# Kernel tuning notes

Measured on AMD Instinct MI355X. Metric: run time of the kernel, lower is better.

## Reference

```python
import jax, jax.numpy as jnp
import numpy as np
import math

D_MODEL, NHEAD, N_LAYERS = 128, 8, 4
LAYER_NAMES = ("self", "cross", "self", "cross")
B, H, W = 2, 128, 160
MID = D_MODEL
D_FF = 2 * D_MODEL
BN_EPS = 1e-5
LN_EPS = 1e-5
ATTN_EPS = 1e-6


def setup_inputs() -> dict:
    key = jax.random.key(0)
    ks = iter(jax.random.split(key, 64))

    def rn(shape, scale):
        return jax.random.normal(next(ks), shape, dtype=jnp.float32) * scale

    inp = {}
    inp["ref_feature"] = rn((B, D_MODEL, H, W), 1.0)
    inp["src_feature"] = rn((B, D_MODEL, H, W), 1.0)
    K = np.array([[200.0, 0.0, W / 2.0], [0.0, 200.0, H / 2.0], [0.0, 0.0, 1.0]], np.float32)

    def make_proj(tx):
        E = np.eye(4, dtype=np.float32); E[0, 3] = tx
        P = np.eye(4, dtype=np.float32); P[:3, :4] = K @ E[:3, :4]
        return np.broadcast_to(P, (B, 4, 4)).astype(np.float32).copy()

    rp, sp = make_proj(0.0), make_proj(10.0)
    inp["ref_proj"] = jnp.asarray(rp)
    inp["src_proj"] = jnp.asarray(sp)
    inp["ref_img2world"] = jnp.asarray(np.linalg.inv(rp))
    inp["src_img2world"] = jnp.asarray(np.linalg.inv(sp))
    inp["depth_hypo"] = 500.0 + 100.0 * jax.random.uniform(next(ks), (B, 1, H, W), dtype=jnp.float32)
    xav = 0.08  # ~xavier std for 128x128
    inp["attn_w"] = rn((N_LAYERS, 4, D_MODEL, D_MODEL), xav)  # q,k,v,out
    inp["attn_b"] = jnp.zeros((N_LAYERS, 4, D_MODEL), jnp.float32)
    inp["ffn_w1"] = rn((N_LAYERS, D_MODEL, D_FF), 0.07)
    inp["ffn_b1"] = jnp.zeros((N_LAYERS, D_FF), jnp.float32)
    inp["ffn_w2"] = rn((N_LAYERS, D_FF, D_MODEL), 0.07)
    inp["ffn_b2"] = jnp.zeros((N_LAYERS, D_MODEL), jnp.float32)
    inp["ln_g"] = jnp.ones((N_LAYERS, 2, D_MODEL), jnp.float32)
    inp["ln_b"] = jnp.zeros((N_LAYERS, 2, D_MODEL), jnp.float32)
    inp["rc_w"] = rn((MID, 1, 3, 3), 0.01)
    inp["rc_b"] = jnp.zeros((MID,), jnp.float32)
    inp["bn2_g"] = jnp.ones((MID,), jnp.float32)
    inp["bn2_b"] = jnp.zeros((MID,), jnp.float32)
    inp["cc_w"] = rn((MID, D_MODEL), xav)
    inp["cc_b"] = jnp.zeros((D_MODEL,), jnp.float32)
    inp["bn1_g"] = jnp.ones((16,), jnp.float32)
    inp["bn1_b"] = jnp.zeros((16,), jnp.float32)
    inp["fc1_w"] = rn((16, MID), 0.16)
    inp["fc1_b"] = jnp.zeros((MID,), jnp.float32)
    inp["fc2_w"] = rn((MID, MID), xav)
    inp["fc2_b"] = jnp.zeros((MID,), jnp.float32)
    inp["ser_w"] = rn((MID, MID), xav)
    inp["ser_b"] = jnp.zeros((MID,), jnp.float32)
    inp["see_w"] = rn((MID, MID), xav)
    inp["see_b"] = jnp.zeros((MID,), jnp.float32)
    return inp


def sine_pe(d_model, Hh, Ww):
    # PositionEncodingSine (temp_bug_fix=True), computed only on the [H,W] slice
    y_pos = jnp.arange(1, Hh + 1, dtype=jnp.float32)[:, None] * jnp.ones((1, Ww), jnp.float32)
    x_pos = jnp.ones((Hh, 1), jnp.float32) * jnp.arange(1, Ww + 1, dtype=jnp.float32)[None, :]
    div = jnp.exp(jnp.arange(0, d_model // 2, 2, dtype=jnp.float32) * (-math.log(10000.0) / (d_model // 2)))[:, None, None]
    pe = jnp.stack([jnp.sin(x_pos * div), jnp.cos(x_pos * div), jnp.sin(y_pos * div), jnp.cos(y_pos * div)], axis=1)
    return pe.reshape(d_model, Hh, Ww)


def grid_sample_bilinear(feat, grid):
    # feat [B,C,Hs,Ws], grid [B,P,2] normalized to [-1,1]; align_corners=True, zeros padding
    Bn, C, Hs, Ws = feat.shape
    P = grid.shape[1]
    x = (grid[..., 0] + 1.0) * 0.5 * (Ws - 1)
    y = (grid[..., 1] + 1.0) * 0.5 * (Hs - 1)
    x0, y0 = jnp.floor(x), jnp.floor(y)
    wx, wy = x - x0, y - y0
    flat = feat.reshape(Bn, C, Hs * Ws)

    def gather(xi, yi):
        valid = (xi >= 0) & (xi <= Ws - 1) & (yi >= 0) & (yi <= Hs - 1)
        xi_c = jnp.clip(xi, 0, Ws - 1).astype(jnp.int32)
        yi_c = jnp.clip(yi, 0, Hs - 1).astype(jnp.int32)
        idx = yi_c * Ws + xi_c  # [B,P]
        v = jnp.take_along_axis(flat, jnp.broadcast_to(idx[:, None, :], (Bn, C, P)), axis=2)
        return v * valid[:, None, :].astype(feat.dtype)

    v00 = gather(x0, y0)
    v01 = gather(x0 + 1, y0)
    v10 = gather(x0, y0 + 1)
    v11 = gather(x0 + 1, y0 + 1)
    wx, wy = wx[:, None, :], wy[:, None, :]
    return v00 * (1 - wx) * (1 - wy) + v01 * wx * (1 - wy) + v10 * (1 - wx) * wy + v11 * wx * wy


def homo_warp_ref_to_src(feat, ref_proj, src_proj, depth):
    # homo_warping_pe with fea='ref': proj = ref_proj @ inv(src_proj)
    Bn, C, Hs, Ws = feat.shape
    _, D, Hr, Wr = depth.shape
    proj = jnp.einsum('bij,bjk->bik', ref_proj, jnp.linalg.inv(src_proj))
    rot, trans = proj[:, :3, :3], proj[:, :3, 3]
    yy, xx = jnp.meshgrid(jnp.arange(Hr, dtype=jnp.float32), jnp.arange(Wr, dtype=jnp.float32), indexing='ij')
    xyz = jnp.stack([xx.ravel(), yy.ravel(), jnp.ones(Hr * Wr, jnp.float32)], 0)  # [3, P]
    rot_xyz = jnp.einsum('bij,jp->bip', rot, xyz)  # [B,3,P]
    pxyz = rot_xyz[:, :, None, :] * depth.reshape(Bn, 1, D, Hr * Wr) + trans[:, :, None, None]
    z = pxyz[:, 2]
    z = jnp.where(z == 0, 1e-9, z)
    gx = (pxyz[:, 0] / z) / ((Ws - 1) / 2.0) - 1.0
    gy = (pxyz[:, 1] / z) / ((Hs - 1) / 2.0) - 1.0
    grid = jax.lax.stop_gradient(jnp.stack([gx, gy], -1).reshape(Bn, D * Hr * Wr, 2))  # torch no_grad
    out = grid_sample_bilinear(feat, grid)
    return out.reshape(Bn, C, D, Hr, Wr)


def layer_norm(x, g, b):
    mu = x.mean(-1, keepdims=True)
    var = ((x - mu) ** 2).mean(-1, keepdims=True)
    return (x - mu) * jax.lax.rsqrt(var + LN_EPS) * g + b


def encoder_layer(x, src, w, bb, w1, b1f, w2, b2f, g, bt):
    N, L, d = x.shape
    h, dh = NHEAD, d // NHEAD
    q = (x @ w[0] + bb[0]).reshape(N, L, h, dh)
    k = (src @ w[1] + bb[1]).reshape(N, -1, h, dh)
    v = (src @ w[2] + bb[2]).reshape(N, -1, h, dh)
    Q = jax.nn.elu(q) + 1.0
    K = jax.nn.elu(k) + 1.0
    KV = jnp.einsum('nshd,nshm->nhmd', K, v)
    Z = 1.0 / (jnp.einsum('nlhd,nhd->nlh', Q, K.sum(1)) + ATTN_EPS)
    V = jnp.einsum('nlhd,nhmd,nlh->nlhm', Q, KV, Z).reshape(N, L, d)
    x = x + (V @ w[3] + bb[3])
    x = layer_norm(x, g[0], bt[0])
    y = jax.nn.relu(x @ w1 + b1f) @ w2 + b2f
    return layer_norm(x + y, g[1], bt[1])


def cam_encode(feat, cam16, rc_w, rc_b, bn2_g, bn2_b, cc_w, cc_b, bn1_g, bn1_b,
               fc1_w, fc1_b, fc2_w, fc2_b, ser_w, ser_b, see_w, see_b):
    inv_std = 1.0 / jnp.sqrt(1.0 + BN_EPS)  # eval-mode BN, running stats (0,1)
    mlp_in = cam16 * inv_std * bn1_g + bn1_b
    hmap = jax.lax.conv_general_dilated(feat, rc_w, (1, 1), 'SAME', dimension_numbers=('NCHW', 'OIHW', 'NCHW')) + rc_b[None, :, None, None]
    hmap = jax.nn.relu(hmap * inv_std * bn2_g[None, :, None, None] + bn2_b[None, :, None, None])
    se = jax.nn.relu(mlp_in @ fc1_w + fc1_b) @ fc2_w + fc2_b  # [B, MID]
    gate = jax.nn.sigmoid(jax.nn.relu(se @ ser_w + ser_b) @ see_w + see_b)
    ctx = hmap * gate[:, :, None, None]
    return jnp.einsum('bchw,co->bohw', ctx, cc_w) + cc_b[None, :, None, None]


def reference(ref_feature, src_feature, ref_img2world, src_img2world, ref_proj, src_proj, depth_hypo,
              attn_w, attn_b, ffn_w1, ffn_b1, ffn_w2, ffn_b2, ln_g, ln_b,
              rc_w, rc_b, bn2_g, bn2_b, cc_w, cc_b, bn1_g, bn1_b,
              fc1_w, fc1_b, fc2_w, fc2_b, ser_w, ser_b, see_w, see_b):
    Bn, C, Hh, Ww = ref_feature.shape
    pe = sine_pe(C, Hh, Ww)[None]
    ref_ctx = cam_encode(depth_hypo, ref_img2world.reshape(Bn, 16), rc_w, rc_b, bn2_g, bn2_b,
                         cc_w, cc_b, bn1_g, bn1_b, fc1_w, fc1_b, fc2_w, fc2_b,
                         ser_w, ser_b, see_w, see_b)
    src_ctx = homo_warp_ref_to_src(ref_ctx, ref_proj, src_proj, depth_hypo)[:, :, 0]
    ref = (ref_feature + pe + ref_ctx).reshape(Bn, C, Hh * Ww).transpose(0, 2, 1)
    src = (src_feature + pe + src_ctx).reshape(Bn, C, Hh * Ww).transpose(0, 2, 1)
    for i, name in enumerate(LAYER_NAMES):
        p = (attn_w[i], attn_b[i], ffn_w1[i], ffn_b1[i], ffn_w2[i], ffn_b2[i], ln_g[i], ln_b[i])
        if name == 'self':
            ref = encoder_layer(ref, ref, *p)
            src = encoder_layer(src, src, *p)
        else:
            ref = encoder_layer(ref, src, *p)
            src = encoder_layer(src, ref, *p)
    return jnp.stack([ref, src])  # [2, B, H*W, C]
```

## Files before the change

kernel.cpp:

```cpp
#include <hip/hip_runtime.h>
#include <math.h>

#define BN 2
#define HH 128
#define WW 160
#define HWn (HH*WW)
#define CD 128
#define TT (BN*HWn)
#define TOKN ((size_t)TT*CD)

typedef __attribute__((ext_vector_type(8))) short bf16x8;
typedef __attribute__((ext_vector_type(4))) float f32x4;
typedef __attribute__((ext_vector_type(4))) unsigned short u16x4;

__device__ __forceinline__ float b2f(unsigned short s){
  unsigned u = ((unsigned)s) << 16;
  return __builtin_bit_cast(float, u);
}
__device__ __forceinline__ unsigned short f2b(float f){
  unsigned u = __builtin_bit_cast(unsigned, f);
  u = (u + 0x7fffu + ((u >> 16) & 1u)) >> 16;
  return (unsigned short)u;
}

__global__ __launch_bounds__(256) void k_wconv(const float* __restrict__ attn_w,
      const float* __restrict__ ffn_w1, const float* __restrict__ ffn_w2,
      const float* __restrict__ cc_w, unsigned short* __restrict__ wt,
      const float* __restrict__ ref_proj, const float* __restrict__ src_i2w,
      const float* __restrict__ cam16,
      const float* __restrict__ bn1_g, const float* __restrict__ bn1_b,
      const float* __restrict__ fc1_w, const float* __restrict__ fc1_b,
      const float* __restrict__ fc2_w, const float* __restrict__ fc2_b,
      const float* __restrict__ ser_w, const float* __restrict__ ser_b,
      const float* __restrict__ see_w, const float* __restrict__ see_b,
      float* __restrict__ projsmall, float* __restrict__ gate){
  if (blockIdx.x == 2112){
    __shared__ float mi[BN][16], t1[BN][128], t2[BN][128];
    int tid = threadIdx.x;
    const float inv_std = rsqrtf(1.0f + 1e-5f);
    if (tid < 32){
      int b = tid >> 4, idx = tid & 15, i = idx >> 2, k = idx & 3;
      float acc = 0.f;
      for (int j = 0; j < 4; j++) acc += ref_proj[b*16 + i*4 + j] * src_i2w[b*16 + j*4 + k];
      if (i < 3 && k < 3) projsmall[b*12 + i*3 + k] = acc;
      if (i < 3 && k == 3) projsmall[b*12 + 9 + i] = acc;
      mi[b][idx] = cam16[b*16 + idx] * inv_std * bn1_g[idx] + bn1_b[idx];
    }
    __syncthreads();
    int b = tid >> 7, c = tid & 127;
    float a = 0.f;
    for (int j = 0; j < 16; j++) a += mi[b][j] * fc1_w[j*128 + c];
    t1[b][c] = fmaxf(a + fc1_b[c], 0.f);
    __syncthreads();
    a = 0.f;
    for (int k = 0; k < 128; k++) a += t1[b][k] * fc2_w[k*128 + c];
    t2[b][c] = a + fc2_b[c];
    __syncthreads();
    a = 0.f;
    for (int k = 0; k < 128; k++) a += t2[b][k] * ser_w[k*128 + c];
    t1[b][c] = fmaxf(a + ser_b[c], 0.f);
    __syncthreads();
    a = 0.f;
    for (int k = 0; k < 128; k++) a += t1[b][k] * see_w[k*128 + c];
    a += see_b[c];
    gate[b*128 + c] = 1.f / (1.f + __expf(-a));
    return;
  }
  int i = blockIdx.x*256 + threadIdx.x;
  float v;
  if (i < 262144){
    int k = i & 127, n = (i >> 7) & 127, lm = i >> 14;
    v = attn_w[((size_t)lm*128 + k)*128 + n];
  } else if (i < 393216){ int j = i - 262144;
    int k = j & 127, n = (j >> 7) & 255, l = j >> 15;
    v = ffn_w1[((size_t)l*128 + k)*256 + n];
  } else if (i < 524288){ int j = i - 393216;
    int k = j & 255, n = (j >> 8) & 127, l = j >> 15;
    v = ffn_w2[((size_t)l*256 + k)*128 + n];
  } else if (i < 540672){ int j = i - 524288;
    int k = j & 127, n = j >> 7;
    v = cc_w[(size_t)k*128 + n];
  } else return;
  wt[i] = f2b(v);
}

__global__ __launch_bounds__(128) void k_hmap(const float* __restrict__ depth,
                       const float* __restrict__ rc_w, const float* __restrict__ rc_b,
                       const float* __restrict__ bn2_g, const float* __restrict__ bn2_b,
                       const float* __restrict__ gate, unsigned short* __restrict__ G){
  int bi = blockIdx.x; int n = bi / HWn; int p = bi - n*HWn;
  int y = p / WW, x = p - y*WW;
  int c = threadIdx.x;
  const float inv_std = rsqrtf(1.f + 1e-5f);
  float acc = 0.f;
#pragma unroll
  for (int ky = 0; ky < 3; ky++){
    int yy = y + ky - 1;
#pragma unroll
    for (int kx = 0; kx < 3; kx++){
      int xx = x + kx - 1;
      float v = (yy >= 0 && yy < HH && xx >= 0 && xx < WW) ? depth[n*HWn + yy*WW + xx] : 0.f;
      acc += v * rc_w[c*9 + ky*3 + kx];
    }
  }
  acc += rc_b[c];
  acc = fmaxf(acc * inv_std * bn2_g[c] + bn2_b[c], 0.f);
  G[(size_t)bi*128 + c] = f2b(acc * gate[n*128 + c]);
}

template<int K, int ACT, int LN>
__global__ __launch_bounds__(256) void k_bgemm6(
    const unsigned short* __restrict__ A, const unsigned short* __restrict__ A2, int ldA,
    const unsigned short* __restrict__ Wt,
    const float* __restrict__ bias, int amask,
    const unsigned short* __restrict__ resid,
    unsigned short* __restrict__ Cbase, size_t secStride, int ldC,
    const float* __restrict__ lng, const float* __restrict__ lnb,
    float* zfin, int zn){
  __shared__ unsigned short Wl[128*128];
  constexpr int NH = K/128;
  int tid = threadIdx.x;
  int wid = tid >> 6, lane = tid & 63;
  int sec = blockIdx.y;
  if (zfin && blockIdx.x == 0 && sec == 0){
    for (int i = tid; i < zn; i += 256) zfin[i] = 0.f;
  }
  const unsigned short* Ab = (sec == 0) ? A : A2;
  const unsigned short* Ws = Wt + (size_t)sec*128*K;
  const float* bs = bias + sec*128;
  unsigned short* C = Cbase + (size_t)sec*secStride;
  int r = lane & 15, ks = lane >> 4;
  size_t t0 = (size_t)blockIdx.x*64 + wid*16;
  const unsigned short* ap = Ab + (t0 + r)*ldA + ks*8;
  f32x4 acc[8] = {};
#pragma unroll
  for (int hh = 0; hh < NH; hh++){
    if (hh > 0) __syncthreads();
#pragma unroll
    for (int i = 0; i < 8; i++){
      int idx = i*256 + tid;
      int row = idx >> 4, c8 = idx & 15;
      int c8s = c8 ^ (row & 7);
      *(bf16x8*)&Wl[row*128 + c8s*8] = *(const bf16x8*)(Ws + (size_t)row*K + hh*128 + c8*8);
    }
    __syncthreads();
#pragma unroll
    for (int j = 0; j < 4; j++){
      bf16x8 a = *(const bf16x8*)(ap + hh*128 + j*32);
#pragma unroll
      for (int f = 0; f < 8; f++){
        int row = f*16 + r;
        int c8s = (j*4 + ks) ^ (row & 7);
        bf16x8 w = *(const bf16x8*)&Wl[row*128 + c8s*8];
        acc[f] = __builtin_amdgcn_mfma_f32_16x16x32_bf16(w, a, acc[f], 0, 0, 0);
      }
    }
  }
  bool act = (amask >> sec) & 1;
  size_t trow = t0 + r;
  float vv[8][4];
#pragma unroll
  for (int f = 0; f < 8; f++){
    float4 bi4 = *(const float4*)&bs[f*16 + 4*ks];
    vv[f][0] = acc[f][0] + bi4.x; vv[f][1] = acc[f][1] + bi4.y;
    vv[f][2] = acc[f][2] + bi4.z; vv[f][3] = acc[f][3] + bi4.w;
    if (resid){
      u16x4 rr = *(const u16x4*)(resid + trow*128 + f*16 + 4*ks);
#pragma unroll
      for (int e = 0; e < 4; e++) vv[f][e] += b2f(rr[e]);
    }
    if (act){
#pragma unroll
      for (int e = 0; e < 4; e++){
        float x = vv[f][e];
        if (ACT == 1) x = fmaxf(x, 0.f);
        if (ACT == 2) x = x > 0.f ? x + 1.f : __expf(x);
        vv[f][e] = x;
      }
    }
  }
  if (LN){
    float s = 0.f;
#pragma unroll
    for (int f = 0; f < 8; f++) s += vv[f][0]+vv[f][1]+vv[f][2]+vv[f][3];
    s += __shfl_xor(s, 16, 64); s += __shfl_xor(s, 32, 64);
    float mean = s * (1.f/128.f);
    float q = 0.f;
#pragma unroll
    for (int f = 0; f < 8; f++)
#pragma unroll
      for (int e = 0; e < 4; e++){ float d = vv[f][e]-mean; q += d*d; }
    q += __shfl_xor(q, 16, 64); q += __shfl_xor(q, 32, 64);
    float rstd = rsqrtf(q*(1.f/128.f) + 1e-5f);
#pragma unroll
    for (int f = 0; f < 8; f++){
      float4 g4 = *(const float4*)&lng[f*16 + 4*ks];
      float4 b4 = *(const float4*)&lnb[f*16 + 4*ks];
      vv[f][0] = (vv[f][0]-mean)*rstd*g4.x + b4.x;
      vv[f][1] = (vv[f][1]-mean)*rstd*g4.y + b4.y;
      vv[f][2] = (vv[f][2]-mean)*rstd*g4.z + b4.z;
      vv[f][3] = (vv[f][3]-mean)*rstd*g4.w + b4.w;
    }
  }
#pragma unroll
  for (int f = 0; f < 8; f++){
    u16x4 o;
#pragma unroll
    for (int e = 0; e < 4; e++) o[e] = f2b(vv[f][e]);
    *(u16x4*)(C + trow*ldC + f*16 + 4*ks) = o;
  }
}

__global__ __launch_bounds__(256) void k_fattnffn(
    const unsigned short* __restrict__ Q, const unsigned short* __restrict__ X,
    const float* __restrict__ kvfin, const unsigned short* __restrict__ W3,
    const float* __restrict__ b3, const float* __restrict__ g0, const float* __restrict__ b0,
    const unsigned short* __restrict__ W1t, const float* __restrict__ b1,
    const unsigned short* __restrict__ W2t, const float* __restrict__ b2,
    const float* __restrict__ g1, const float* __restrict__ lb1,
    unsigned short* __restrict__ Out, float* __restrict__ OutF){
  __shared__ unsigned short Wl[128*128];
  __shared__ unsigned short UB[64*136];
  __shared__ float ksums[8][16];
  int tid = threadIdx.x;
  size_t tb = (size_t)blockIdx.x*64;
  int g = (int)(tb / HWn);
  const float* kvb = kvfin + g*2176;
  {
    int row = tid >> 1, half = tid & 1;
    int h = row >> 4, m = row & 15;
    int swz = row & 7;
#pragma unroll
    for (int c8i = 0; c8i < 8; c8i++){
      int c8 = half*8 + c8i;
      bf16x8 val = {};
      if ((c8 >> 1) == h){
        int d0 = (c8 & 1)*8;
        const float* src = kvb + h*272 + m*16 + d0;
#pragma unroll
        for (int e = 0; e < 8; e++) ((unsigned short*)&val)[e] = f2b(src[e]);
      }
      *(bf16x8*)&Wl[row*128 + (c8 ^ swz)*8] = val;
    }
  }
  if (tid < 128) ksums[tid >> 4][tid & 15] = kvb[(tid >> 4)*272 + 256 + (tid & 15)];
  __syncthreads();
  int wid = tid >> 6, lane = tid & 63;
  int r = lane & 15, ks = lane >> 4;
  int tl = wid*16 + r;
  size_t trow = tb + tl;
  f32x4 acc[8] = {};
  float part0 = 0.f, part1 = 0.f, part2 = 0.f, part3 = 0.f;
  int myp = ks >> 1;
  int dlo = (ks & 1)*8;
#pragma unroll
  for (int j = 0; j < 4; j++){
    bf16x8 a = *(const bf16x8*)(Q + trow*128 + j*32 + ks*8);
    float pj = 0.f;
    int hj = 2*j + myp;
#pragma unroll
    for (int e = 0; e < 8; e++)
      pj += b2f(((unsigned short*)&a)[e]) * ksums[hj][dlo + e];
    if (j == 0) part0 = pj; else if (j == 1) part1 = pj;
    else if (j == 2) part2 = pj; else part3 = pj;
#pragma unroll
    for (int f = 0; f < 8; f++){
      int row = f*16 + r;
      int c8s = (j*4 + ks) ^ (row & 7);
      bf16x8 w = *(const bf16x8*)&Wl[row*128 + c8s*8];
      acc[f] = __builtin_amdgcn_mfma_f32_16x16x32_bf16(w, a, acc[f], 0, 0, 0);
    }
  }
  float full0 = part0 + __shfl_xor(part0, 16, 64);
  float full1 = part1 + __shfl_xor(part1, 16, 64);
  float full2 = part2 + __shfl_xor(part2, 16, 64);
  float full3 = part3 + __shfl_xor(part3, 16, 64);
  float oth0 = __shfl_xor(full0, 32, 64);
  float oth1 = __shfl_xor(full1, 32, 64);
  float oth2 = __shfl_xor(full2, 32, 64);
  float oth3 = __shfl_xor(full3, 32, 64);
#pragma unroll
  for (int f = 0; f < 8; f++){
    float fl, ot;
    if (f < 2){ fl = full0; ot = oth0; } else if (f < 4){ fl = full1; ot = oth1; }
    else if (f < 6){ fl = full2; ot = oth2; } else { fl = full3; ot = oth3; }
    float den = ((f & 1) == myp) ? fl : ot;
    float rc = 1.f / (den + 1e-6f);
    u16x4 o;
#pragma unroll
    for (int e = 0; e < 4; e++) o[e] = f2b(acc[f][e] * rc);
    *(u16x4*)&UB[tl*136 + f*16 + 4*ks] = o;
  }
  __syncthreads();
#pragma unroll
  for (int i = 0; i < 8; i++){
    int idx = i*256 + tid;
    int row = idx >> 4, c8 = idx & 15;
    int c8s = c8 ^ (row & 7);
    *(bf16x8*)&Wl[row*128 + c8s*8] = *(const bf16x8*)(W3 + (size_t)row*128 + c8*8);
  }
  __syncthreads();
  f32x4 acc2[8] = {};
#pragma unroll
  for (int j = 0; j < 4; j++){
    bf16x8 a = *(const bf16x8*)&UB[tl*136 + j*32 + ks*8];
#pragma unroll
    for (int f = 0; f < 8; f++){
      int row = f*16 + r;
      int c8s = (j*4 + ks) ^ (row & 7);
      bf16x8 w = *(const bf16x8*)&Wl[row*128 + c8s*8];
      acc2[f] = __builtin_amdgcn_mfma_f32_16x16x32_bf16(w, a, acc2[f], 0, 0, 0);
    }
  }
  float vv[8][4];
#pragma unroll
  for (int f = 0; f < 8; f++){
    float4 bi4 = *(const float4*)&b3[f*16 + 4*ks];
    u16x4 rr = *(const u16x4*)(X + trow*128 + f*16 + 4*ks);
    vv[f][0] = acc2[f][0] + bi4.x + b2f(rr[0]);
    vv[f][1] = acc2[f][1] + bi4.y + b2f(rr[1]);
    vv[f][2] = acc2[f][2] + bi4.z + b2f(rr[2]);
    vv[f][3] = acc2[f][3] + bi4.w + b2f(rr[3]);
  }
  {
    float s = 0.f;
#pragma unroll
    for (int f = 0; f < 8; f++) s += vv[f][0]+vv[f][1]+vv[f][2]+vv[f][3];
    s += __shfl_xor(s, 16, 64); s += __shfl_xor(s, 32, 64);
    float mean = s * (1.f/128.f);
    float q = 0.f;
#pragma unroll
    for (int f = 0; f < 8; f++)
#pragma unroll
      for (int e = 0; e < 4; e++){ float d = vv[f][e]-mean; q += d*d; }
    q += __shfl_xor(q, 16, 64); q += __shfl_xor(q, 32, 64);
    float rstd = rsqrtf(q*(1.f/128.f) + 1e-5f);
#pragma unroll
    for (int f = 0; f < 8; f++){
      float4 g4 = *(const float4*)&g0[f*16 + 4*ks];
      float4 b4 = *(const float4*)&b0[f*16 + 4*ks];
      vv[f][0] = (vv[f][0]-mean)*rstd*g4.x + b4.x;
      vv[f][1] = (vv[f][1]-mean)*rstd*g4.y + b4.y;
      vv[f][2] = (vv[f][2]-mean)*rstd*g4.z + b4.z;
      vv[f][3] = (vv[f][3]-mean)*rstd*g4.w + b4.w;
    }
  }
  u16x4 xr[8];
#pragma unroll
  for (int f = 0; f < 8; f++){
#pragma unroll
    for (int e = 0; e < 4; e++) xr[f][e] = f2b(vv[f][e]);
    *(u16x4*)&UB[tl*136 + f*16 + 4*ks] = xr[f];
  }
  __syncthreads();
  bf16x8 areg[4];
#pragma unroll
  for (int j = 0; j < 4; j++) areg[j] = *(const bf16x8*)&UB[tl*136 + j*32 + ks*8];
  f32x4 acc3[8] = {};
#pragma unroll
  for (int hh = 0; hh < 2; hh++){
    if (hh > 0) __syncthreads();
#pragma unroll
    for (int i = 0; i < 8; i++){
      int idx = i*256 + tid;
      int row = idx >> 4, c8 = idx & 15;
      *(bf16x8*)&Wl[row*128 + (c8 ^ (row & 7))*8] =
          *(const bf16x8*)(W1t + (size_t)(hh*128 + row)*128 + c8*8);
    }
    __syncthreads();
    f32x4 accf[8] = {};
#pragma unroll
    for (int j = 0; j < 4; j++){
#pragma unroll
      for (int f = 0; f < 8; f++){
        int row = f*16 + r;
        int c8s = (j*4 + ks) ^ (row & 7);
        bf16x8 w = *(const bf16x8*)&Wl[row*128 + c8s*8];
        accf[f] = __builtin_amdgcn_mfma_f32_16x16x32_bf16(w, areg[j], accf[f], 0, 0, 0);
      }
    }
#pragma unroll
    for (int f = 0; f < 8; f++){
      float4 bi4 = *(const float4*)&b1[hh*128 + f*16 + 4*ks];
      u16x4 o;
      o[0] = f2b(fmaxf(accf[f][0] + bi4.x, 0.f));
      o[1] = f2b(fmaxf(accf[f][1] + bi4.y, 0.f));
      o[2] = f2b(fmaxf(accf[f][2] + bi4.z, 0.f));
      o[3] = f2b(fmaxf(accf[f][3] + bi4.w, 0.f));
      *(u16x4*)&UB[tl*136 + f*16 + 4*ks] = o;
    }
    __syncthreads();
#pragma unroll
    for (int i = 0; i < 8; i++){
      int idx = i*256 + tid;
      int row = idx >> 4, c8 = idx & 15;
      *(bf16x8*)&Wl[row*128 + (c8 ^ (row & 7))*8] =
          *(const bf16x8*)(W2t + (size_t)row*256 + hh*128 + c8*8);
    }
    __syncthreads();
#pragma unroll
    for (int j = 0; j < 4; j++){
      bf16x8 a = *(const bf16x8*)&UB[tl*136 + j*32 + ks*8];
#pragma unroll
      for (int f = 0; f < 8; f++){
        int row = f*16 + r;
        int c8s = (j*4 + ks) ^ (row & 7);
        bf16x8 w = *(const bf16x8*)&Wl[row*128 + c8s*8];
        acc3[f] = __builtin_amdgcn_mfma_f32_16x16x32_bf16(w, a, acc3[f], 0, 0, 0);
      }
    }
  }
#pragma unroll
  for (int f = 0; f < 8; f++){
    float4 bi4 = *(const float4*)&b2[f*16 + 4*ks];
    vv[f][0] = acc3[f][0] + bi4.x + b2f(xr[f][0]);
    vv[f][1] = acc3[f][1] + bi4.y + b2f(xr[f][1]);
    vv[f][2] = acc3[f][2] + bi4.z + b2f(xr[f][2]);
    vv[f][3] = acc3[f][3] + bi4.w + b2f(xr[f][3]);
  }
  float s = 0.f;
#pragma unroll
  for (int f = 0; f < 8; f++) s += vv[f][0]+vv[f][1]+vv[f][2]+vv[f][3];
  s += __shfl_xor(s, 16, 64); s += __shfl_xor(s, 32, 64);
  float mean = s * (1.f/128.f);
  float q = 0.f;
#pragma unroll
  for (int f = 0; f < 8; f++)
#pragma unroll
    for (int e = 0; e < 4; e++){ float d = vv[f][e]-mean; q += d*d; }
  q += __shfl_xor(q, 16, 64); q += __shfl_xor(q, 32, 64);
  float rstd = rsqrtf(q*(1.f/128.f) + 1e-5f);
#pragma unroll
  for (int f = 0; f < 8; f++){
    float o0 = (vv[f][0]-mean)*rstd* g1[f*16 + 4*ks + 0] + lb1[f*16 + 4*ks + 0];
    float o1 = (vv[f][1]-mean)*rstd* g1[f*16 + 4*ks + 1] + lb1[f*16 + 4*ks + 1];
    float o2 = (vv[f][2]-mean)*rstd* g1[f*16 + 4*ks + 2] + lb1[f*16 + 4*ks + 2];
    float o3 = (vv[f][3]-mean)*rstd* g1[f*16 + 4*ks + 3] + lb1[f*16 + 4*ks + 3];
    if (Out){
      u16x4 o = { f2b(o0), f2b(o1), f2b(o2), f2b(o3) };
      *(u16x4*)(Out + trow*128 + f*16 + 4*ks) = o;
    }
    if (OutF){
      float4 of = { o0, o1, o2, o3 };
      *(float4*)(OutF + trow*128 + f*16 + 4*ks) = of;
    }
  }
}

__global__ __launch_bounds__(256) void k_kvpart(const unsigned short* __restrict__ Kb,
                         const unsigned short* __restrict__ Vb, float* __restrict__ fin){
  __shared__ float Ks[16][260], Vs[16][260];
  int bi = blockIdx.x;
  int chunk = bi % 80; int h = (bi / 80) & 7; int g = bi / 640;
  int s0 = chunk * 256;
  int tid = threadIdx.x;
#pragma unroll
  for (int rr = 0; rr < 8; rr++){
    int idx = rr*256 + tid;
    int s = idx >> 3, d2 = idx & 7;
    size_t gg = ((size_t)(g*HWn + s0 + s))*128 + h*16 + d2*2;
    Ks[d2*2  ][s] = b2f(Kb[gg]);
    Ks[d2*2+1][s] = b2f(Kb[gg+1]);
    Vs[d2*2  ][s] = b2f(Vb[gg]);
    Vs[d2*2+1][s] = b2f(Vb[gg+1]);
  }
  __syncthreads();
  int m = tid >> 4, d = tid & 15;
  float acc = 0.f, ksum = 0.f;
#pragma unroll 4
  for (int s4 = 0; s4 < 64; s4++){
    float4 kv = *(const float4*)&Ks[d][s4*4];
    float4 vv = *(const float4*)&Vs[m][s4*4];
    acc  += kv.x*vv.x + kv.y*vv.y + kv.z*vv.z + kv.w*vv.w;
    ksum += kv.x + kv.y + kv.z + kv.w;
  }
  float* fb = fin + (size_t)(g*8 + h)*272;
  atomicAdd(&fb[tid], acc);
  if (m == 0) atomicAdd(&fb[256 + d], ksum);
}

__global__ __launch_bounds__(128) void k_warp(const unsigned short* __restrict__ ctxref,
     const float* __restrict__ depth, const float* __restrict__ projs,
     unsigned short* __restrict__ ctxsrc){
  int bi = blockIdx.x; int n = bi / HWn; int p = bi - n*HWn;
  int y = p / WW, x = p - y*WW;
  const float* pr = &projs[n*12];
  float d = depth[n*HWn + p];
  float fx = (float)x, fy = (float)y;
  float px = (pr[0]*fx + pr[1]*fy + pr[2])*d + pr[9];
  float py = (pr[3]*fx + pr[4]*fy + pr[5])*d + pr[10];
  float pz = (pr[6]*fx + pr[7]*fy + pr[8])*d + pr[11];
  if (pz == 0.f) pz = 1e-9f;
  float xs = px/pz, ys = py/pz;
  float x0 = floorf(xs), y0 = floorf(ys);
  float wx = xs - x0, wy = ys - y0;
  int c = threadIdx.x;
  float acc = 0.f;
#pragma unroll
  for (int dy = 0; dy < 2; dy++){
    float cy = y0 + dy;
    float wyv = dy ? wy : 1.f - wy;
#pragma unroll
    for (int dx = 0; dx < 2; dx++){
      float cx = x0 + dx;
      float wxv = dx ? wx : 1.f - wx;
      bool valid = (cx >= 0.f) && (cx <= (float)(WW-1)) && (cy >= 0.f) && (cy <= (float)(HH-1));
      int xi = (int)fminf(fmaxf(cx, 0.f), (float)(WW-1));
      int yi = (int)fminf(fmaxf(cy, 0.f), (float)(HH-1));
      float v = b2f(ctxref[((size_t)(n*HWn) + yi*WW + xi)*128 + c]);
      acc += valid ? wxv*wyv*v : 0.f;
    }
  }
  ctxsrc[(size_t)bi*128 + c] = f2b(acc);
}

__global__ __launch_bounds__(256) void k_build2(const float* __restrict__ featR,
      const float* __restrict__ featS,
      const unsigned short* __restrict__ ctxR, const unsigned short* __restrict__ ctxS,
      unsigned short* __restrict__ outR, unsigned short* __restrict__ outS){
  __shared__ float tile[32][33];
  int tx = threadIdx.x, ty = threadIdx.y;
  int z = blockIdx.z; int b = z & (BN-1); int sel = z >> 1;
  const float* feat = sel ? featS : featR;
  const unsigned short* ctx = sel ? ctxS : ctxR;
  unsigned short* out = sel ? outS : outR;
  int p0 = blockIdx.x*32, c0 = blockIdx.y*32;
  for (int i = ty; i < 32; i += 8)
    tile[i][tx] = feat[((size_t)(b*CD + c0 + i))*HWn + p0 + tx];
  __syncthreads();
  const float LOG1E4_32 = 0.28782313662425572f;
  for (int r = ty; r < 32; r += 8){
    int p = p0 + r, c = c0 + tx;
    int y = p / WW, x = p - y*WW;
    int i = c >> 2, j = c & 3;
    float dv = __expf(-(float)i * LOG1E4_32);
    float pos = (j < 2) ? (float)(x + 1) : (float)(y + 1);
    float arg = pos * dv;
    float pe = (j & 1) ? cosf(arg) : sinf(arg);
    size_t o = ((size_t)(b*HWn) + p)*128 + c;
    out[o] = f2b(tile[tx][r] + pe + b2f(ctx[o]));
  }
}

extern "C" void kernel_launch(void* const* d_in, const int* in_sizes, int n_in,
                              void* d_out, int out_size, void* d_ws, size_t ws_size,
                              hipStream_t stream) {
  const float* ref_feature = (const float*)d_in[0];
  const float* src_feature = (const float*)d_in[1];
  const float* ref_proj    = (const float*)d_in[2];
  const float* ref_i2w     = (const float*)d_in[4];
  const float* src_i2w     = (const float*)d_in[5];
  const float* depth       = (const float*)d_in[6];
  const float* attn_w      = (const float*)d_in[7];
  const float* attn_b      = (const float*)d_in[8];
  const float* ffn_w1      = (const float*)d_in[9];
  const float* ffn_b1      = (const float*)d_in[10];
  const float* ffn_w2      = (const float*)d_in[11];
  const float* ffn_b2      = (const float*)d_in[12];
  const float* ln_g        = (const float*)d_in[13];
  const float* ln_b        = (const float*)d_in[14];
  const float* rc_w        = (const float*)d_in[15];
  const float* rc_b        = (const float*)d_in[16];
  const float* bn2_g       = (const float*)d_in[17];
  const float* bn2_b       = (const float*)d_in[18];
  const float* cc_w        = (const float*)d_in[19];
  const float* cc_b        = (const float*)d_in[20];
  const float* bn1_g       = (const float*)d_in[21];
  const float* bn1_b       = (const float*)d_in[22];
  const float* fc1_w       = (const float*)d_in[23];
  const float* fc1_b       = (const float*)d_in[24];
  const float* fc2_w       = (const float*)d_in[25];
  const float* fc2_b       = (const float*)d_in[26];
  const float* ser_w       = (const float*)d_in[27];
  const float* ser_b       = (const float*)d_in[28];
  const float* see_w       = (const float*)d_in[29];
  const float* see_b       = (const float*)d_in[30];

  const size_t small_f32 = (size_t)4*2176 + 32 + 256;
  const size_t small_bytes = small_f32*4 + (size_t)540672*2 + 4096;
  const size_t need_batch = (size_t)TOKN*2*8 + small_bytes;
  bool BATCH = ws_size >= need_batch;
  const size_t CSEG = BATCH ? 2*TOKN : TOKN;

  char* p = (char*)d_ws;
  unsigned short* Rm = (unsigned short*)p; p += TOKN*2;
  unsigned short* Sm = (unsigned short*)p; p += TOKN*2;
  unsigned short* QB = (unsigned short*)p; p += CSEG*3*2;
  unsigned short* KB = QB + CSEG;
  unsigned short* VB = QB + 2*CSEG;
  float* KVFIN  = (float*)p; p += (size_t)(BATCH?4:2)*2176*4;
  float* PROJ   = (float*)p; p += 32*4;
  float* GATE   = (float*)p; p += 256*4;
  unsigned short* WT = (unsigned short*)p;

  float* OUT = (float*)d_out;

  k_wconv<<<2113, 256, 0, stream>>>(attn_w, ffn_w1, ffn_w2, cc_w, WT,
      ref_proj, src_i2w, ref_i2w, bn1_g, bn1_b, fc1_w, fc1_b,
      fc2_w, fc2_b, ser_w, ser_b, see_w, see_b, PROJ, GATE);
  k_hmap<<<TT, 128, 0, stream>>>(depth, rc_w, rc_b, bn2_g, bn2_b, GATE, QB);
  k_bgemm6<128,0,0><<<dim3(TT/64, 1), 256, 0, stream>>>(
      QB, QB, 128, WT + 524288, cc_b, 0, nullptr, KB, 0, 128, nullptr, nullptr,
      nullptr, 0);
  k_warp<<<TT, 128, 0, stream>>>(KB, depth, PROJ, VB);
  k_build2<<<dim3(HWn/32, 4, 2*BN), dim3(32, 8), 0, stream>>>(
      ref_feature, src_feature, KB, VB, Rm, Sm);

  auto encode = [&](unsigned short* x, const unsigned short* srcp, int l, int nTok,
                    unsigned short* outBf, float* outF){
    const unsigned short* ATW = WT + (size_t)l*65536;
    const unsigned short* F1T = WT + 262144 + (size_t)l*32768;
    const unsigned short* F2T = WT + 393216 + (size_t)l*32768;
    const float* Bv = attn_b + (size_t)l*512;
    const float* g0 = ln_g + (size_t)l*256; const float* b0 = ln_b + (size_t)l*256;
    int nb = nTok/64, ng = nTok/HWn;
    k_bgemm6<128,2,0><<<dim3(nb, 3), 256, 0, stream>>>(x, srcp, 128, ATW, Bv, 0b011,
                                              nullptr, QB, CSEG, 128, nullptr, nullptr,
                                              KVFIN, ng*2176);
    k_kvpart<<<ng*640, 256, 0, stream>>>(KB, VB, KVFIN);
    k_fattnffn<<<nb, 256, 0, stream>>>(QB, x, KVFIN, ATW + 3*16384, Bv + 384, g0, b0,
                                       F1T, ffn_b1 + (size_t)l*256, F2T,
                                       ffn_b2 + (size_t)l*128, g0 + 128, b0 + 128,
                                       outBf, outF);
  };

  if (BATCH) encode(Rm, Rm, 0, 2*TT, Rm, nullptr);
  else { encode(Rm, Rm, 0, TT, Rm, nullptr); encode(Sm, Sm, 0, TT, Sm, nullptr); }
  encode(Rm, Sm, 1, TT, Rm, nullptr); encode(Sm, Rm, 1, TT, Sm, nullptr);
  if (BATCH) encode(Rm, Rm, 2, 2*TT, Rm, nullptr);
  else { encode(Rm, Rm, 2, TT, Rm, nullptr); encode(Sm, Sm, 2, TT, Sm, nullptr); }
  encode(Rm, Sm, 3, TT, Rm, OUT);
  encode(Sm, Rm, 3, TT, nullptr, OUT + TOKN);
}
```

Measured before the change: 551.8 us.

## Fuse QKV projection with KV reduction and double-buffer KV accumulator zeroing

Replaces the three-section QKV GEMM and separate kvpart reduction with one kernel. It computes Q, K and V per 64-token tile, keeps K and V in shared memory, and atomically accumulates the per-head K^T V and K sums. This removes writing and re-reading the K/V buffers and saves a launch per layer. The KV accumulator is now double-buffered and zeroed by the previous attention/FFN kernel, with the initial zeroing done in the weight-conversion kernel. The trade-off is more serialized work per block and contention from many global atomics.

```diff
diff --git a/kernel.cpp b/kernel.cpp
--- a/kernel.cpp
+++ b/kernel.cpp
@@ -33,7 +33,12 @@
       const float* __restrict__ fc2_w, const float* __restrict__ fc2_b,
       const float* __restrict__ ser_w, const float* __restrict__ ser_b,
       const float* __restrict__ see_w, const float* __restrict__ see_b,
-      float* __restrict__ projsmall, float* __restrict__ gate){
+      float* __restrict__ projsmall, float* __restrict__ gate,
+      float* __restrict__ kvz, int kvn){
+  if (blockIdx.x == 2113){
+    for (int i = threadIdx.x; i < kvn; i += 256) kvz[i] = 0.f;
+    return;
+  }
   if (blockIdx.x == 2112){
     __shared__ float mi[BN][16], t1[BN][128], t2[BN][128];
     int tid = threadIdx.x;
@@ -115,16 +120,12 @@
     const float* __restrict__ bias, int amask,
     const unsigned short* __restrict__ resid,
     unsigned short* __restrict__ Cbase, size_t secStride, int ldC,
-    const float* __restrict__ lng, const float* __restrict__ lnb,
-    float* zfin, int zn){
+    const float* __restrict__ lng, const float* __restrict__ lnb){
   __shared__ unsigned short Wl[128*128];
   constexpr int NH = K/128;
   int tid = threadIdx.x;
   int wid = tid >> 6, lane = tid & 63;
   int sec = blockIdx.y;
-  if (zfin && blockIdx.x == 0 && sec == 0){
-    for (int i = tid; i < zn; i += 256) zfin[i] = 0.f;
-  }
   const unsigned short* Ab = (sec == 0) ? A : A2;
   const unsigned short* Ws = Wt + (size_t)sec*128*K;
   const float* bs = bias + sec*128;
@@ -211,6 +212,144 @@
   }
 }
 
+__global__ __launch_bounds__(256) void k_qkv(
+    const unsigned short* __restrict__ X, const unsigned short* __restrict__ S,
+    const unsigned short* __restrict__ Wt,
+    const float* __restrict__ bias,
+    unsigned short* __restrict__ QB, float* __restrict__ kvfin){
+  __shared__ unsigned short Wl[128*128];
+  __shared__ unsigned short Kl[64*136];
+  int tid = threadIdx.x;
+  int wid = tid >> 6, lane = tid & 63;
+  int r = lane & 15, ks = lane >> 4;
+  size_t t0 = (size_t)blockIdx.x*64 + wid*16;
+  int tl = wid*16 + r;
+  size_t trow = t0 + r;
+  int g = (int)(((size_t)blockIdx.x*64) / HWn);
+  bf16x8 ax[4], as_[4];
+#pragma unroll
+  for (int j = 0; j < 4; j++){
+    ax[j]  = *(const bf16x8*)(X + trow*128 + j*32 + ks*8);
+    as_[j] = *(const bf16x8*)(S + trow*128 + j*32 + ks*8);
+  }
+#pragma unroll
+  for (int i = 0; i < 8; i++){
+    int idx = i*256 + tid;
+    int row = idx >> 4, c8 = idx & 15;
+    *(bf16x8*)&Wl[row*128 + (c8 ^ (row & 7))*8] = *(const bf16x8*)(Wt + (size_t)row*128 + c8*8);
+  }
+  __syncthreads();
+  {
+    f32x4 acc[8] = {};
+#pragma unroll
+    for (int j = 0; j < 4; j++)
+#pragma unroll
+      for (int f = 0; f < 8; f++){
+        int row = f*16 + r;
+        bf16x8 w = *(const bf16x8*)&Wl[row*128 + ((j*4 + ks) ^ (row & 7))*8];
+        acc[f] = __builtin_amdgcn_mfma_f32_16x16x32_bf16(w, ax[j], acc[f], 0, 0, 0);
+      }
+    __syncthreads();
+#pragma unroll
+    for (int i = 0; i < 8; i++){
+      int idx = i*256 + tid;
+      int row = idx >> 4, c8 = idx & 15;
+      *(bf16x8*)&Wl[row*128 + (c8 ^ (row & 7))*8] =
+          *(const bf16x8*)(Wt + 16384 + (size_t)row*128 + c8*8);
+    }
+#pragma unroll
+    for (int f = 0; f < 8; f++){
+      float4 b4 = *(const float4*)&bias[f*16 + 4*ks];
+      u16x4 o;
+#pragma unroll
+      for (int e = 0; e < 4; e++){
+        float x = acc[f][e] + ((const float*)&b4)[e];
+        x = x > 0.f ? x + 1.f : __expf(x);
+        o[e] = f2b(x);
+      }
+      *(u16x4*)(QB + trow*128 + f*16 + 4*ks) = o;
+    }
+  }
+  __syncthreads();
+  {
+    f32x4 acc[8] = {};
+#pragma unroll
+    for (int j = 0; j < 4; j++)
+#pragma unroll
+      for (int f = 0; f < 8; f++){
+        int row = f*16 + r;
+        bf16x8 w = *(const bf16x8*)&Wl[row*128 + ((j*4 + ks) ^ (row & 7))*8];
+        acc[f] = __builtin_amdgcn_mfma_f32_16x16x32_bf16(w, as_[j], acc[f], 0, 0, 0);
+      }
+    __syncthreads();
+#pragma unroll
+    for (int i = 0; i < 8; i++){
+      int idx = i*256 + tid;
+      int row = idx >> 4, c8 = idx & 15;
+      *(bf16x8*)&Wl[row*128 + (c8 ^ (row & 7))*8] =
+          *(const bf16x8*)(Wt + 32768 + (size_t)row*128 + c8*8);
+    }
+#pragma unroll
+    for (int f = 0; f < 8; f++){
+      float4 b4 = *(const float4*)&bias[128 + f*16 + 4*ks];
+      u16x4 o;
+#pragma unroll
+      for (int e = 0; e < 4; e++){
+        float x = acc[f][e] + ((const float*)&b4)[e];
+        x = x > 0.f ? x + 1.f : __expf(x);
+        o[e] = f2b(x);
+      }
+      *(u16x4*)&Kl[tl*136 + f*16 + 4*ks] = o;
+    }
+  }
+  __syncthreads();
+  {
+    f32x4 acc[8] = {};
+#pragma unroll
+    for (int j = 0; j < 4; j++)
+#pragma unroll
+      for (int f = 0; f < 8; f++){
+        int row = f*16 + r;
+        bf16x8 w = *(const bf16x8*)&Wl[row*128 + ((j*4 + ks) ^ (row & 7))*8];
+        acc[f] = __builtin_amdgcn_mfma_f32_16x16x32_bf16(w, as_[j], acc[f], 0, 0, 0);
+      }
+    __syncthreads();
+    unsigned short* Vl = Wl;
+#pragma unroll
+    for (int f = 0; f < 8; f++){
+      float4 b4 = *(const float4*)&bias[256 + f*16 + 4*ks];
+      u16x4 o;
+#pragma unroll
+      for (int e = 0; e < 4; e++) o[e] = f2b(acc[f][e] + ((const float*)&b4)[e]);
+      *(u16x4*)&Vl[tl*136 + f*16 + 4*ks] = o;
+    }
+  }
+  __syncthreads();
+  {
+    const unsigned short* Vl = Wl;
+    int h = tid >> 5, m = (tid >> 1) & 15, db = (tid & 1)*8;
+    float a8[8] = {}; float ksc[8] = {};
+#pragma unroll 4
+    for (int t = 0; t < 64; t++){
+      float vv_ = b2f(Vl[t*136 + h*16 + m]);
+      bf16x8 kk = *(const bf16x8*)&Kl[t*136 + h*16 + db];
+#pragma unroll
+      for (int c = 0; c < 8; c++){
+        float kf = b2f(((unsigned short*)&kk)[c]);
+        a8[c] += kf * vv_;
+        ksc[c] += kf;
+      }
+    }
+    float* fb = kvfin + (size_t)g*2176 + h*272;
+#pragma unroll
+    for (int c = 0; c < 8; c++) atomicAdd(fb + m*16 + db + c, a8[c]);
+    if (m == 0){
+#pragma unroll
+      for (int c = 0; c < 8; c++) atomicAdd(fb + 256 + db + c, ksc[c]);
+    }
+  }
+}
+
 __global__ __launch_bounds__(256) void k_fattnffn(
     const unsigned short* __restrict__ Q, const unsigned short* __restrict__ X,
     const float* __restrict__ kvfin, const unsigned short* __restrict__ W3,
@@ -218,11 +357,15 @@
     const unsigned short* __restrict__ W1t, const float* __restrict__ b1,
     const unsigned short* __restrict__ W2t, const float* __restrict__ b2,
     const float* __restrict__ g1, const float* __restrict__ lb1,
-    unsigned short* __restrict__ Out, float* __restrict__ OutF){
+    unsigned short* __restrict__ Out, float* __restrict__ OutF,
+    float* zeroNext, int zn){
   __shared__ unsigned short Wl[128*128];
   __shared__ unsigned short UB[64*136];
   __shared__ float ksums[8][16];
   int tid = threadIdx.x;
+  if (zeroNext && blockIdx.x == 0){
+    for (int i = tid; i < zn; i += 256) zeroNext[i] = 0.f;
+  }
   size_t tb = (size_t)blockIdx.x*64;
   int g = (int)(tb / HWn);
   const float* kvb = kvfin + g*2176;
@@ -432,10 +575,12 @@
   float rstd = rsqrtf(q*(1.f/128.f) + 1e-5f);
 #pragma unroll
   for (int f = 0; f < 8; f++){
-    float o0 = (vv[f][0]-mean)*rstd* g1[f*16 + 4*ks + 0] + lb1[f*16 + 4*ks + 0];
-    float o1 = (vv[f][1]-mean)*rstd* g1[f*16 + 4*ks + 1] + lb1[f*16 + 4*ks + 1];
-    float o2 = (vv[f][2]-mean)*rstd* g1[f*16 + 4*ks + 2] + lb1[f*16 + 4*ks + 2];
-    float o3 = (vv[f][3]-mean)*rstd* g1[f*16 + 4*ks + 3] + lb1[f*16 + 4*ks + 3];
+    float4 g4 = *(const float4*)&g1[f*16 + 4*ks];
+    float4 b4 = *(const float4*)&lb1[f*16 + 4*ks];
+    float o0 = (vv[f][0]-mean)*rstd*g4.x + b4.x;
+    float o1 = (vv[f][1]-mean)*rstd*g4.y + b4.y;
+    float o2 = (vv[f][2]-mean)*rstd*g4.z + b4.z;
+    float o3 = (vv[f][3]-mean)*rstd*g4.w + b4.w;
     if (Out){
       u16x4 o = { f2b(o0), f2b(o1), f2b(o2), f2b(o3) };
       *(u16x4*)(Out + trow*128 + f*16 + 4*ks) = o;
@@ -445,38 +590,6 @@
       *(float4*)(OutF + trow*128 + f*16 + 4*ks) = of;
     }
   }
-}
-
-__global__ __launch_bounds__(256) void k_kvpart(const unsigned short* __restrict__ Kb,
-                         const unsigned short* __restrict__ Vb, float* __restrict__ fin){
-  __shared__ float Ks[16][260], Vs[16][260];
-  int bi = blockIdx.x;
-  int chunk = bi % 80; int h = (bi / 80) & 7; int g = bi / 640;
-  int s0 = chunk * 256;
-  int tid = threadIdx.x;
-#pragma unroll
-  for (int rr = 0; rr < 8; rr++){
-    int idx = rr*256 + tid;
-    int s = idx >> 3, d2 = idx & 7;
-    size_t gg = ((size_t)(g*HWn + s0 + s))*128 + h*16 + d2*2;
-    Ks[d2*2  ][s] = b2f(Kb[gg]);
-    Ks[d2*2+1][s] = b2f(Kb[gg+1]);
-    Vs[d2*2  ][s] = b2f(Vb[gg]);
-    Vs[d2*2+1][s] = b2f(Vb[gg+1]);
-  }
-  __syncthreads();
-  int m = tid >> 4, d = tid & 15;
-  float acc = 0.f, ksum = 0.f;
-#pragma unroll 4
-  for (int s4 = 0; s4 < 64; s4++){
-    float4 kv = *(const float4*)&Ks[d][s4*4];
-    float4 vv = *(const float4*)&Vs[m][s4*4];
-    acc  += kv.x*vv.x + kv.y*vv.y + kv.z*vv.z + kv.w*vv.w;
-    ksum += kv.x + kv.y + kv.z + kv.w;
-  }
-  float* fb = fin + (size_t)(g*8 + h)*272;
-  atomicAdd(&fb[tid], acc);
-  if (m == 0) atomicAdd(&fb[256 + d], ksum);
 }
 
 __global__ __launch_bounds__(128) void k_warp(const unsigned short* __restrict__ ctxref,
@@ -576,7 +689,7 @@
   const float* see_w       = (const float*)d_in[29];
   const float* see_b       = (const float*)d_in[30];
 
-  const size_t small_f32 = (size_t)4*2176 + 32 + 256;
+  const size_t small_f32 = (size_t)2*4*2176 + 32 + 256;
   const size_t small_bytes = small_f32*4 + (size_t)540672*2 + 4096;
   const size_t need_batch = (size_t)TOKN*2*8 + small_bytes;
   bool BATCH = ws_size >= need_batch;
@@ -588,24 +701,25 @@
   unsigned short* QB = (unsigned short*)p; p += CSEG*3*2;
   unsigned short* KB = QB + CSEG;
   unsigned short* VB = QB + 2*CSEG;
-  float* KVFIN  = (float*)p; p += (size_t)(BATCH?4:2)*2176*4;
+  float* KVFIN  = (float*)p; p += (size_t)2*4*2176*4;
   float* PROJ   = (float*)p; p += 32*4;
   float* GATE   = (float*)p; p += 256*4;
   unsigned short* WT = (unsigned short*)p;
 
   float* OUT = (float*)d_out;
 
-  k_wconv<<<2113, 256, 0, stream>>>(attn_w, ffn_w1, ffn_w2, cc_w, WT,
+  k_wconv<<<2114, 256, 0, stream>>>(attn_w, ffn_w1, ffn_w2, cc_w, WT,
       ref_proj, src_i2w, ref_i2w, bn1_g, bn1_b, fc1_w, fc1_b,
-      fc2_w, fc2_b, ser_w, ser_b, see_w, see_b, PROJ, GATE);
+      fc2_w, fc2_b, ser_w, ser_b, see_w, see_b, PROJ, GATE,
+      KVFIN, 2*4*2176);
   k_hmap<<<TT, 128, 0, stream>>>(depth, rc_w, rc_b, bn2_g, bn2_b, GATE, QB);
   k_bgemm6<128,0,0><<<dim3(TT/64, 1), 256, 0, stream>>>(
-      QB, QB, 128, WT + 524288, cc_b, 0, nullptr, KB, 0, 128, nullptr, nullptr,
-      nullptr, 0);
+      QB, QB, 128, WT + 524288, cc_b, 0, nullptr, KB, 0, 128, nullptr, nullptr);
   k_warp<<<TT, 128, 0, stream>>>(KB, depth, PROJ, VB);
   k_build2<<<dim3(HWn/32, 4, 2*BN), dim3(32, 8), 0, stream>>>(
       ref_feature, src_feature, KB, VB, Rm, Sm);
 
+  int eidx = 0;
   auto encode = [&](unsigned short* x, const unsigned short* srcp, int l, int nTok,
                     unsigned short* outBf, float* outF){
     const unsigned short* ATW = WT + (size_t)l*65536;
@@ -613,15 +727,15 @@
     const unsigned short* F2T = WT + 393216 + (size_t)l*32768;
     const float* Bv = attn_b + (size_t)l*512;
     const float* g0 = ln_g + (size_t)l*256; const float* b0 = ln_b + (size_t)l*256;
-    int nb = nTok/64, ng = nTok/HWn;
-    k_bgemm6<128,2,0><<<dim3(nb, 3), 256, 0, stream>>>(x, srcp, 128, ATW, Bv, 0b011,
-                                              nullptr, QB, CSEG, 128, nullptr, nullptr,
-                                              KVFIN, ng*2176);
-    k_kvpart<<<ng*640, 256, 0, stream>>>(KB, VB, KVFIN);
-    k_fattnffn<<<nb, 256, 0, stream>>>(QB, x, KVFIN, ATW + 3*16384, Bv + 384, g0, b0,
+    int nb = nTok/64;
+    float* kvCur = KVFIN + (size_t)(eidx & 1)*4*2176;
+    float* kvNxt = KVFIN + (size_t)((eidx + 1) & 1)*4*2176;
+    eidx++;
+    k_qkv<<<nb, 256, 0, stream>>>(x, srcp, ATW, Bv, QB, kvCur);
+    k_fattnffn<<<nb, 256, 0, stream>>>(QB, x, kvCur, ATW + 3*16384, Bv + 384, g0, b0,
                                        F1T, ffn_b1 + (size_t)l*256, F2T,
                                        ffn_b2 + (size_t)l*128, g0 + 128, b0 + 128,
-                                       outBf, outF);
+                                       outBf, outF, kvNxt, 4*2176);
   };
 
   if (BATCH) encode(Rm, Rm, 0, 2*TT, Rm, nullptr);
```

New measurement: 1.116 ms. 102% more time.
